# Kernel tuning notes

Measured on AMD Instinct MI355X. Metric: run time of the kernel, lower is better.

The kernel has to match this reference:

```python
import jax, jax.numpy as jnp
import numpy as np

S, B, C, H, E = 4096, 2, 256, 8, 131072
CC = C // H


def setup_inputs() -> dict:
    key = jax.random.key(0)
    ks = jax.random.split(key, 12)
    sc = 0.02
    inp = {
        "x": jax.random.normal(ks[0], (S, B, C), jnp.float32),
        "q_id": jax.random.randint(ks[1], (E,), 0, S, jnp.int32),
        "k_id": jax.random.randint(ks[2], (E,), 0, S, jnp.int32),
        "Wq": jax.random.normal(ks[3], (C, C), jnp.float32) * sc,
        "bq": jnp.zeros((C,), jnp.float32),
        "Wk": jax.random.normal(ks[4], (C, C), jnp.float32) * sc,
        "bk": jnp.zeros((C,), jnp.float32),
        "Wv": jax.random.normal(ks[5], (C, C), jnp.float32) * sc,
        "bv": jnp.zeros((C,), jnp.float32),
        "Wx": jax.random.normal(ks[6], (C, C), jnp.float32) * sc,
        "bx": jnp.zeros((C,), jnp.float32),
    }
    return inp


def reference(x, q_id, k_id, Wq, bq, Wk, bk, Wv, bv, Wx, bx):
    s, b, c = x.shape
    cc = c // H
    # qkv projections (torch Linear: x @ W.T + b)
    q = (x @ Wq.T + bq).reshape(s, b, H, cc)
    k = (x @ Wk.T + bk).reshape(s, b, H, cc)
    v = (x @ Wv.T + bv).reshape(s, b, H, cc)
    # per-edge scores: gather along sequence axis by edge ids
    qk = jnp.einsum('ebhc,ebhc->ebh', q[q_id], k[k_id])[..., None]  # [E,b,h,1]
    qk = qk / jnp.sqrt(jnp.asarray(cc, x.dtype))
    eqk = jnp.exp(qk - jnp.max(qk))  # global max, as in original
    # scatter-add softmax normalizer and weighted sum over edges
    d = jnp.zeros((s, b, H, 1), x.dtype).at[q_id].add(eqk)
    out = jnp.zeros((s, b, H, cc), x.dtype).at[q_id].add(eqk * v[k_id])
    out = (out / d).reshape(s, b, c)
    return out @ Wx.T + bx
```

## Files before the change

kernel.cpp:

```cpp
#include <hip/hip_runtime.h>

constexpr int S_  = 4096;
constexpr int B_  = 2;
constexpr int C_  = 256;
constexpr int H_  = 8;
constexpr int E_  = 131072;
constexpr int CC_ = 32;
constexpr int MR  = S_ * B_;

typedef __attribute__((ext_vector_type(8))) short bf16x8_t;
typedef __attribute__((ext_vector_type(4))) float f32x4_t;

__device__ __forceinline__ unsigned short f2bf(float f) {
    unsigned int u = __float_as_uint(f);
    u += 0x7fffu + ((u >> 16) & 1u);
    return (unsigned short)(u >> 16);
}
__device__ __forceinline__ float bflo(unsigned int u) { return __uint_as_float(u << 16); }
__device__ __forceinline__ float bfhi(unsigned int u) { return __uint_as_float(u & 0xffff0000u); }

__device__ __forceinline__ void cast8(const float* __restrict__ src, unsigned short* __restrict__ dst, int i) {
    const float4* s = (const float4*)src + (size_t)i * 2;
    float4 a = s[0], b = s[1];
    uint4 o;
    o.x = (unsigned)f2bf(a.x) | ((unsigned)f2bf(a.y) << 16);
    o.y = (unsigned)f2bf(a.z) | ((unsigned)f2bf(a.w) << 16);
    o.z = (unsigned)f2bf(b.x) | ((unsigned)f2bf(b.y) << 16);
    o.w = (unsigned)f2bf(b.z) | ((unsigned)f2bf(b.w) << 16);
    *((uint4*)dst + i) = o;
}


__global__ __launch_bounds__(256) void prep_kernel(
        const int* __restrict__ q_id, int* __restrict__ count,
        const float* __restrict__ x, unsigned short* __restrict__ xb,
        const float* __restrict__ Wq, const float* __restrict__ Wk,
        const float* __restrict__ Wv, const float* __restrict__ Wx,
        unsigned short* __restrict__ Wb) {
    const int bid = blockIdx.x, tid = threadIdx.x;
    if (bid < 512) {
        atomicAdd(&count[q_id[bid * 256 + tid]], 1);
    } else if (bid < 1536) {
        cast8(x, xb, (bid - 512) * 256 + tid);
    } else {
        int idx = bid - 1536;
        int z = idx >> 5;
        const float* src = (z == 0) ? Wq : (z == 1) ? Wk : (z == 2) ? Wv : Wx;
        cast8(src, Wb + (size_t)z * (C_ * C_), (idx & 31) * 256 + tid);
    }
}


__global__ __launch_bounds__(1024) void scan_kernel(const int* __restrict__ count,
                                                    int* __restrict__ base,
                                                    int* __restrict__ cursor) {
    __shared__ int wsums[16];
    const int t = threadIdx.x, lane = t & 63, w = t >> 6;
    int c0 = count[4 * t + 0], c1 = count[4 * t + 1];
    int c2 = count[4 * t + 2], c3 = count[4 * t + 3];
    int tsum = c0 + c1 + c2 + c3;
    int x = tsum;
#pragma unroll
    for (int off = 1; off < 64; off <<= 1) {
        int y = __shfl_up(x, off);
        if (lane >= off) x += y;
    }
    if (lane == 63) wsums[w] = x;
    __syncthreads();
    if (t == 0) {
        int run = 0;
#pragma unroll
        for (int i = 0; i < 16; ++i) { int v = wsums[i]; wsums[i] = run; run += v; }
        base[S_] = run;
    }
    __syncthreads();
    int excl = x - tsum + wsums[w];
    int b0 = excl, b1 = b0 + c0, b2 = b1 + c1, b3 = b2 + c2;
    base[4 * t + 0] = b0; base[4 * t + 1] = b1;
    base[4 * t + 2] = b2; base[4 * t + 3] = b3;
    cursor[4 * t + 0] = b0; cursor[4 * t + 1] = b1;
    cursor[4 * t + 2] = b2; cursor[4 * t + 3] = b3;
}


__global__ __launch_bounds__(256) void scatter_qkv_kernel(
        const int* __restrict__ q_id, const int* __restrict__ k_id,
        int* __restrict__ cursor, int* __restrict__ koff_sorted,
        const unsigned short* __restrict__ xb, const unsigned short* __restrict__ Wb,
        const float* __restrict__ bq, const float* __restrict__ bk, const float* __restrict__ bv,
        unsigned short* __restrict__ qb, unsigned short* __restrict__ kvb) {
    __shared__ __align__(16) unsigned short As[64][264];
    const int bid = blockIdx.x, tid = threadIdx.x;
    if (bid < 512) {
        int e = bid * 256 + tid;
        int pos = atomicAdd(&cursor[q_id[e]], 1);
        koff_sorted[pos] = k_id[e] << 10;
        return;
    }
    const int u = bid - 512;
    const int nb = u % 12, mg = u / 12;
    const int lane = tid & 63, wave = tid >> 6;
    const int l16 = lane & 15, quad = lane >> 4;
    const int z = nb >> 2;
    const int colz = ((nb & 3) << 6) + (wave << 4);

    const unsigned short* Wrow = Wb + (size_t)z * (C_ * C_) + (size_t)(colz + l16) * C_;
    bf16x8_t breg[8];
#pragma unroll
    for (int ks = 0; ks < 8; ++ks)
        breg[ks] = *(const bf16x8_t*)(Wrow + ks * 32 + quad * 8);

    const float* bias = (z == 0) ? bq : (z == 1) ? bk : bv;
    const float bcol = bias[colz + l16];
    unsigned short* ob = (z == 0) ? qb : kvb;
    const int ostr = (z == 0) ? 256 : 512;
    const int ocol = ((z == 2) ? 256 : 0) + colz + l16;

    const int c0 = (mg * 128) / 43, c1 = ((mg + 1) * 128) / 43;
    for (int c = c0; c < c1; ++c) {
        const int mbase = c * 64;
        __syncthreads();
#pragma unroll
        for (int it = 0; it < 8; ++it) {
            int l = it * 256 + tid;
            int r = l >> 5, cc = (l & 31) << 3;
            *(uint4*)&As[r][cc] = *(const uint4*)&xb[(size_t)(mbase + r) * C_ + cc];
        }
        __syncthreads();
#pragma unroll
        for (int mt = 0; mt < 4; ++mt) {
            f32x4_t acc = {0.f, 0.f, 0.f, 0.f};
#pragma unroll
            for (int ks = 0; ks < 8; ++ks) {
                bf16x8_t a = *(const bf16x8_t*)&As[mt * 16 + l16][ks * 32 + quad * 8];
                acc = __builtin_amdgcn_mfma_f32_16x16x32_bf16(a, breg[ks], acc, 0, 0, 0);
            }
            const int row0 = mbase + mt * 16 + quad * 4;
#pragma unroll
            for (int r = 0; r < 4; ++r)
                ob[(size_t)(row0 + r) * ostr + ocol] = f2bf(acc[r] + bcol);
        }
    }
}


__global__ __launch_bounds__(256) void attn_edge(
        const unsigned short* __restrict__ qb, const unsigned short* __restrict__ kvb,
        const int* __restrict__ base, const int* __restrict__ koff,
        unsigned short* __restrict__ attnb) {
    __shared__ float red[2][64][9];
    const int lane = threadIdx.x & 63;
    const int wave = threadIdx.x >> 6;
    const int rw = wave >> 1, part = wave & 1;
    const int s = blockIdx.x * 2 + rw;
    const int half = lane >> 5, hl = lane & 31;
    const int e0 = __builtin_amdgcn_readfirstlane(base[s]);
    const int e1 = __builtin_amdgcn_readfirstlane(base[s + 1]);

    const uint4 qq = *((const uint4*)(qb + (size_t)(s * 2 + half) * C_) + hl);
    const float q0 = bflo(qq.x), q1 = bfhi(qq.x), q2 = bflo(qq.y), q3 = bfhi(qq.y);
    const float q4 = bflo(qq.z), q5 = bfhi(qq.z), q6 = bflo(qq.w), q7 = bfhi(qq.w);

    float a0 = 0.f, a1 = 0.f, a2 = 0.f, a3 = 0.f, a4 = 0.f, a5 = 0.f, a6 = 0.f, a7 = 0.f;
    float wsum = 0.f;
    const float scale = 0.17677669529663687f;

    auto edge = [&](const uint4& kk, const uint4& vv) {
        float p = q0 * bflo(kk.x) + q1 * bfhi(kk.x)
                + q2 * bflo(kk.y) + q3 * bfhi(kk.y)
                + q4 * bflo(kk.z) + q5 * bfhi(kk.z)
                + q6 * bflo(kk.w) + q7 * bfhi(kk.w);
        p += __shfl_xor(p, 1);
        p += __shfl_xor(p, 2);
        const float w = __expf(p * scale);
        a0 = fmaf(w, bflo(vv.x), a0); a1 = fmaf(w, bfhi(vv.x), a1);
        a2 = fmaf(w, bflo(vv.y), a2); a3 = fmaf(w, bfhi(vv.y), a3);
        a4 = fmaf(w, bflo(vv.z), a4); a5 = fmaf(w, bfhi(vv.z), a5);
        a6 = fmaf(w, bflo(vv.w), a6); a7 = fmaf(w, bfhi(vv.w), a7);
        wsum += w;
    };
    auto fetch = [&](int my, int t, uint4& kk, uint4& vv) {
        int o = __builtin_amdgcn_readlane(my, part + 2 * t);
        const uint4* p = (const uint4*)(kvb + o + half * 512);
        kk = p[hl]; vv = p[32 + hl];
    };

    for (int b0 = e0; b0 < e1; b0 += 64) {
        const int m = min(64, e1 - b0);
        const int my = koff[b0 + ((lane < m) ? lane : 0)];
        const int nm = (m > part) ? ((m - part + 1) >> 1) : 0;
        uint4 kka = {}, vva = {}, kkb = {}, vvb = {};
        if (nm > 0) fetch(my, 0, kka, vva);
        if (nm > 1) fetch(my, 1, kkb, vvb);
        int t = 0;
        for (; t + 3 < nm; t += 2) {
            edge(kka, vva);
            fetch(my, t + 2, kka, vva);
            edge(kkb, vvb);
            fetch(my, t + 3, kkb, vvb);
        }
        if (t < nm)     edge(kka, vva);
        if (t + 1 < nm) edge(kkb, vvb);
        if (t + 2 < nm) { fetch(my, t + 2, kka, vva); edge(kka, vva); }
    }

    if (part == 1) {
        float* r = red[rw][lane];
        r[0] = a0; r[1] = a1; r[2] = a2; r[3] = a3;
        r[4] = a4; r[5] = a5; r[6] = a6; r[7] = a7; r[8] = wsum;
    }
    __syncthreads();
    if (part == 0) {
        const float* r = red[rw][lane];
        a0 += r[0]; a1 += r[1]; a2 += r[2]; a3 += r[3];
        a4 += r[4]; a5 += r[5]; a6 += r[6]; a7 += r[7]; wsum += r[8];
        const float inv = 1.0f / wsum;
        uint4 o;
        o.x = (unsigned)f2bf(a0 * inv) | ((unsigned)f2bf(a1 * inv) << 16);
        o.y = (unsigned)f2bf(a2 * inv) | ((unsigned)f2bf(a3 * inv) << 16);
        o.z = (unsigned)f2bf(a4 * inv) | ((unsigned)f2bf(a5 * inv) << 16);
        o.w = (unsigned)f2bf(a6 * inv) | ((unsigned)f2bf(a7 * inv) << 16);
        *((uint4*)(attnb + (size_t)(s * 2 + half) * C_) + hl) = o;
    }
}


__global__ __launch_bounds__(256) void gemm_proj(
        const unsigned short* __restrict__ attnb, const unsigned short* __restrict__ Wxb,
        const float* __restrict__ bx, float* __restrict__ out) {
    __shared__ __align__(16) unsigned short As[64][264];
    const int tid = threadIdx.x;
    const int nb = blockIdx.x & 3, mg = blockIdx.x >> 2;
    const int lane = tid & 63, wave = tid >> 6;
    const int l16 = lane & 15, quad = lane >> 4;
    const int colz = (nb << 6) + (wave << 4);

    const unsigned short* Wrow = Wxb + (size_t)(colz + l16) * C_;
    bf16x8_t breg[8];
#pragma unroll
    for (int ks = 0; ks < 8; ++ks)
        breg[ks] = *(const bf16x8_t*)(Wrow + ks * 32 + quad * 8);
    const float bcol = bx[colz + l16];
    const int ocol = colz + l16;

    const int mbase = mg * 64;
#pragma unroll
    for (int it = 0; it < 8; ++it) {
        int l = it * 256 + tid;
        int r = l >> 5, cc = (l & 31) << 3;
        *(uint4*)&As[r][cc] = *(const uint4*)&attnb[(size_t)(mbase + r) * C_ + cc];
    }
    __syncthreads();
#pragma unroll
    for (int mt = 0; mt < 4; ++mt) {
        f32x4_t acc = {0.f, 0.f, 0.f, 0.f};
#pragma unroll
        for (int ks = 0; ks < 8; ++ks) {
            bf16x8_t a = *(const bf16x8_t*)&As[mt * 16 + l16][ks * 32 + quad * 8];
            acc = __builtin_amdgcn_mfma_f32_16x16x32_bf16(a, breg[ks], acc, 0, 0, 0);
        }
        const int row0 = mbase + mt * 16 + quad * 4;
#pragma unroll
        for (int r = 0; r < 4; ++r)
            out[(size_t)(row0 + r) * C_ + ocol] = acc[r] + bcol;
    }
}


extern "C" void kernel_launch(void* const* d_in, const int* in_sizes, int n_in,
                              void* d_out, int out_size, void* d_ws, size_t ws_size,
                              hipStream_t stream) {
    const float* x  = (const float*)d_in[0];
    const int* q_id = (const int*)d_in[1];
    const int* k_id = (const int*)d_in[2];
    const float* Wq = (const float*)d_in[3];
    const float* bq = (const float*)d_in[4];
    const float* Wk = (const float*)d_in[5];
    const float* bk = (const float*)d_in[6];
    const float* Wv = (const float*)d_in[7];
    const float* bv = (const float*)d_in[8];
    const float* Wx = (const float*)d_in[9];
    const float* bx = (const float*)d_in[10];
    float* out = (float*)d_out;

    char* ws = (char*)d_ws;
    unsigned short* xb    = (unsigned short*)ws;                 ws += (size_t)MR * C_ * 2;
    unsigned short* qb    = (unsigned short*)ws;                 ws += (size_t)MR * C_ * 2;
    unsigned short* kvb   = (unsigned short*)ws;                 ws += (size_t)MR * 512 * 2;
    unsigned short* attnb = (unsigned short*)ws;                 ws += (size_t)MR * C_ * 2;
    unsigned short* Wb    = (unsigned short*)ws;                 ws += (size_t)4 * C_ * C_ * 2;
    int* count       = (int*)ws;                                 ws += S_ * 4;
    int* base        = (int*)ws;                                 ws += (S_ + 1) * 4;
    int* cursor      = (int*)ws;                                 ws += S_ * 4;
    int* koff_sorted = (int*)ws;

    hipMemsetAsync(count, 0, S_ * sizeof(int), stream);
    prep_kernel<<<1664, 256, 0, stream>>>(q_id, count, x, xb, Wq, Wk, Wv, Wx, Wb);
    scan_kernel<<<1, 1024, 0, stream>>>(count, base, cursor);
    scatter_qkv_kernel<<<1028, 256, 0, stream>>>(q_id, k_id, cursor, koff_sorted,
                                                 xb, Wb, bq, bk, bv, qb, kvb);
    attn_edge<<<S_ / 2, 256, 0, stream>>>(qb, kvb, base, koff_sorted, attnb);
    gemm_proj<<<512, 256, 0, stream>>>(attnb, Wb + (size_t)3 * C_ * C_, bx, out);
}
```

Before: 147.6 us.

## Store K in FP8, split K/V buffers, four waves per node in edge attention

Keys are now written in FP8 into their own buffer, and V gets a separate bf16 buffer, which shrinks the gathered K traffic per edge. The attention kernel now gives each sequence node one block of four waves instead of two waves. Each wave computes up to 16 edge weights first and then gathers V in a second pass, with a three-way shared-memory reduction at the end. The scan kernel is also reshaped to 256 threads with 16 elements each. FP8 keys add quantisation error to the attention scores, and the 16-entry weight array raises register pressure.

```diff
diff --git a/kernel.cpp b/kernel.cpp
--- a/kernel.cpp
+++ b/kernel.cpp
@@ -18,6 +18,44 @@
 }
 __device__ __forceinline__ float bflo(unsigned int u) { return __uint_as_float(u << 16); }
 __device__ __forceinline__ float bfhi(unsigned int u) { return __uint_as_float(u & 0xffff0000u); }
+
+__device__ __forceinline__ unsigned char f2fp8(float f) {
+#if __has_builtin(__builtin_amdgcn_cvt_pk_fp8_f32)
+    return (unsigned char)(__builtin_amdgcn_cvt_pk_fp8_f32(f, f, 0, false) & 0xff);
+#else
+    unsigned u = __float_as_uint(f);
+    unsigned s = (u >> 31) << 7;
+    int e = (int)((u >> 23) & 0xff) - 127;
+    unsigned m = u & 0x7fffff;
+    if (e < -9) return (unsigned char)s;
+    if (e < -6) {
+        float a = __uint_as_float(u & 0x7fffffff);
+        unsigned q = (unsigned)__float2int_rn(a * 512.0f);
+        return (unsigned char)(s | q);
+    }
+    unsigned mr = (m + 0x7ffffu + ((m >> 20) & 1u)) >> 20;
+    if (mr >= 8) { mr = 0; ++e; }
+    if (e > 8) return (unsigned char)(s | 0x7e);
+    return (unsigned char)(s | ((unsigned)(e + 7) << 3) | mr);
+#endif
+}
+
+__device__ __forceinline__ void fp8x4_dec(unsigned w, float* d) {
+#if __has_builtin(__builtin_amdgcn_cvt_pk_f32_fp8)
+    auto lo = __builtin_amdgcn_cvt_pk_f32_fp8((int)w, false);
+    auto hi = __builtin_amdgcn_cvt_pk_f32_fp8((int)w, true);
+    d[0] = lo[0]; d[1] = lo[1]; d[2] = hi[0]; d[3] = hi[1];
+#else
+#pragma unroll
+    for (int i = 0; i < 4; ++i) {
+        unsigned b = (w >> (8 * i)) & 0xffu;
+        unsigned s = b >> 7, e = (b >> 3) & 15u, m = b & 7u;
+        float v = e ? __uint_as_float(((e + 120u) << 23) | (m << 20))
+                    : (float)m * 0.001953125f;
+        d[i] = s ? -v : v;
+    }
+#endif
+}
 
 __device__ __forceinline__ void cast8(const float* __restrict__ src, unsigned short* __restrict__ dst, int i) {
     const float4* s = (const float4*)src + (size_t)i * 2;
@@ -51,15 +89,15 @@
 }
 
 
-__global__ __launch_bounds__(1024) void scan_kernel(const int* __restrict__ count,
-                                                    int* __restrict__ base,
-                                                    int* __restrict__ cursor) {
-    __shared__ int wsums[16];
+__global__ __launch_bounds__(256) void scan_kernel(const int* __restrict__ count,
+                                                   int* __restrict__ base,
+                                                   int* __restrict__ cursor) {
+    __shared__ int wsums[4];
     const int t = threadIdx.x, lane = t & 63, w = t >> 6;
-    int c0 = count[4 * t + 0], c1 = count[4 * t + 1];
-    int c2 = count[4 * t + 2], c3 = count[4 * t + 3];
-    int tsum = c0 + c1 + c2 + c3;
-    int x = tsum;
+    int c[16]; int s = 0;
+#pragma unroll
+    for (int i = 0; i < 16; ++i) { c[i] = count[t * 16 + i]; s += c[i]; }
+    int x = s;
 #pragma unroll
     for (int off = 1; off < 64; off <<= 1) {
         int y = __shfl_up(x, off);
@@ -70,89 +108,100 @@
     if (t == 0) {
         int run = 0;
 #pragma unroll
-        for (int i = 0; i < 16; ++i) { int v = wsums[i]; wsums[i] = run; run += v; }
+        for (int i = 0; i < 4; ++i) { int v = wsums[i]; wsums[i] = run; run += v; }
         base[S_] = run;
     }
     __syncthreads();
-    int excl = x - tsum + wsums[w];
-    int b0 = excl, b1 = b0 + c0, b2 = b1 + c1, b3 = b2 + c2;
-    base[4 * t + 0] = b0; base[4 * t + 1] = b1;
-    base[4 * t + 2] = b2; base[4 * t + 3] = b3;
-    cursor[4 * t + 0] = b0; cursor[4 * t + 1] = b1;
-    cursor[4 * t + 2] = b2; cursor[4 * t + 3] = b3;
+    int run = x - s + wsums[w];
+#pragma unroll
+    for (int i = 0; i < 16; ++i) {
+        base[t * 16 + i] = run; cursor[t * 16 + i] = run; run += c[i];
+    }
+}
+
+
+__device__ __forceinline__ void qkv_unit(
+        int u, int tid,
+        const unsigned short* __restrict__ xb, const unsigned short* __restrict__ Wb,
+        const float* __restrict__ bq, const float* __restrict__ bk, const float* __restrict__ bv,
+        unsigned short* __restrict__ qb, unsigned char* __restrict__ kf8,
+        unsigned short* __restrict__ vb, unsigned short (*As)[264]) {
+    const int nb = u % 12, mg = u / 12;
+    const int lane = tid & 63, wave = tid >> 6;
+    const int l16 = lane & 15, quad = lane >> 4;
+    const int z = nb >> 2;
+    const int colz = ((nb & 3) << 6) + (wave << 4);
+
+    const unsigned short* Wrow = Wb + (size_t)z * (C_ * C_) + (size_t)(colz + l16) * C_;
+    bf16x8_t breg[8];
+#pragma unroll
+    for (int ks = 0; ks < 8; ++ks)
+        breg[ks] = *(const bf16x8_t*)(Wrow + ks * 32 + quad * 8);
+
+    const float* bias = (z == 0) ? bq : (z == 1) ? bk : bv;
+    const float bcol = bias[colz + l16];
+    unsigned short* obb = (z == 0) ? qb : vb;
+    const int ocol = colz + l16;
+
+    const int c0 = (mg * 128) / 43, c1 = ((mg + 1) * 128) / 43;
+    for (int c = c0; c < c1; ++c) {
+        const int mbase = c * 64;
+        __syncthreads();
+#pragma unroll
+        for (int it = 0; it < 8; ++it) {
+            int l = it * 256 + tid;
+            int r = l >> 5, cc = (l & 31) << 3;
+            *(uint4*)&As[r][cc] = *(const uint4*)&xb[(size_t)(mbase + r) * C_ + cc];
+        }
+        __syncthreads();
+#pragma unroll
+        for (int mt = 0; mt < 4; ++mt) {
+            f32x4_t acc = {0.f, 0.f, 0.f, 0.f};
+#pragma unroll
+            for (int ks = 0; ks < 8; ++ks) {
+                bf16x8_t a = *(const bf16x8_t*)&As[mt * 16 + l16][ks * 32 + quad * 8];
+                acc = __builtin_amdgcn_mfma_f32_16x16x32_bf16(a, breg[ks], acc, 0, 0, 0);
+            }
+            const int row0 = mbase + mt * 16 + quad * 4;
+#pragma unroll
+            for (int r = 0; r < 4; ++r) {
+                float val = acc[r] + bcol;
+                if (z == 1) kf8[(size_t)(row0 + r) * 256 + ocol] = f2fp8(val);
+                else        obb[(size_t)(row0 + r) * 256 + ocol] = f2bf(val);
+            }
+        }
+    }
 }
 
 
 __global__ __launch_bounds__(256) void scatter_qkv_kernel(
         const int* __restrict__ q_id, const int* __restrict__ k_id,
-        int* __restrict__ cursor, int* __restrict__ koff_sorted,
+        int* __restrict__ cursor, int* __restrict__ koff,
         const unsigned short* __restrict__ xb, const unsigned short* __restrict__ Wb,
         const float* __restrict__ bq, const float* __restrict__ bk, const float* __restrict__ bv,
-        unsigned short* __restrict__ qb, unsigned short* __restrict__ kvb) {
+        unsigned short* __restrict__ qb, unsigned char* __restrict__ kf8,
+        unsigned short* __restrict__ vb) {
     __shared__ __align__(16) unsigned short As[64][264];
     const int bid = blockIdx.x, tid = threadIdx.x;
     if (bid < 512) {
         int e = bid * 256 + tid;
         int pos = atomicAdd(&cursor[q_id[e]], 1);
-        koff_sorted[pos] = k_id[e] << 10;
+        koff[pos] = k_id[e] << 9;
         return;
     }
-    const int u = bid - 512;
-    const int nb = u % 12, mg = u / 12;
-    const int lane = tid & 63, wave = tid >> 6;
-    const int l16 = lane & 15, quad = lane >> 4;
-    const int z = nb >> 2;
-    const int colz = ((nb & 3) << 6) + (wave << 4);
-
-    const unsigned short* Wrow = Wb + (size_t)z * (C_ * C_) + (size_t)(colz + l16) * C_;
-    bf16x8_t breg[8];
-#pragma unroll
-    for (int ks = 0; ks < 8; ++ks)
-        breg[ks] = *(const bf16x8_t*)(Wrow + ks * 32 + quad * 8);
-
-    const float* bias = (z == 0) ? bq : (z == 1) ? bk : bv;
-    const float bcol = bias[colz + l16];
-    unsigned short* ob = (z == 0) ? qb : kvb;
-    const int ostr = (z == 0) ? 256 : 512;
-    const int ocol = ((z == 2) ? 256 : 0) + colz + l16;
-
-    const int c0 = (mg * 128) / 43, c1 = ((mg + 1) * 128) / 43;
-    for (int c = c0; c < c1; ++c) {
-        const int mbase = c * 64;
-        __syncthreads();
-#pragma unroll
-        for (int it = 0; it < 8; ++it) {
-            int l = it * 256 + tid;
-            int r = l >> 5, cc = (l & 31) << 3;
-            *(uint4*)&As[r][cc] = *(const uint4*)&xb[(size_t)(mbase + r) * C_ + cc];
-        }
-        __syncthreads();
-#pragma unroll
-        for (int mt = 0; mt < 4; ++mt) {
-            f32x4_t acc = {0.f, 0.f, 0.f, 0.f};
-#pragma unroll
-            for (int ks = 0; ks < 8; ++ks) {
-                bf16x8_t a = *(const bf16x8_t*)&As[mt * 16 + l16][ks * 32 + quad * 8];
-                acc = __builtin_amdgcn_mfma_f32_16x16x32_bf16(a, breg[ks], acc, 0, 0, 0);
-            }
-            const int row0 = mbase + mt * 16 + quad * 4;
-#pragma unroll
-            for (int r = 0; r < 4; ++r)
-                ob[(size_t)(row0 + r) * ostr + ocol] = f2bf(acc[r] + bcol);
-        }
-    }
+    qkv_unit(bid - 512, tid, xb, Wb, bq, bk, bv, qb, kf8, vb, As);
 }
 
 
 __global__ __launch_bounds__(256) void attn_edge(
-        const unsigned short* __restrict__ qb, const unsigned short* __restrict__ kvb,
+        const unsigned short* __restrict__ qb, const unsigned char* __restrict__ kf8,
+        const unsigned short* __restrict__ vb,
         const int* __restrict__ base, const int* __restrict__ koff,
         unsigned short* __restrict__ attnb) {
-    __shared__ float red[2][64][9];
+    __shared__ float red[3][64][9];
     const int lane = threadIdx.x & 63;
-    const int wave = threadIdx.x >> 6;
-    const int rw = wave >> 1, part = wave & 1;
-    const int s = blockIdx.x * 2 + rw;
+    const int part = threadIdx.x >> 6;
+    const int s = blockIdx.x;
     const int half = lane >> 5, hl = lane & 31;
     const int e0 = __builtin_amdgcn_readfirstlane(base[s]);
     const int e1 = __builtin_amdgcn_readfirstlane(base[s + 1]);
@@ -164,56 +213,58 @@
     float a0 = 0.f, a1 = 0.f, a2 = 0.f, a3 = 0.f, a4 = 0.f, a5 = 0.f, a6 = 0.f, a7 = 0.f;
     float wsum = 0.f;
     const float scale = 0.17677669529663687f;
-
-    auto edge = [&](const uint4& kk, const uint4& vv) {
-        float p = q0 * bflo(kk.x) + q1 * bfhi(kk.x)
-                + q2 * bflo(kk.y) + q3 * bfhi(kk.y)
-                + q4 * bflo(kk.z) + q5 * bfhi(kk.z)
-                + q6 * bflo(kk.w) + q7 * bfhi(kk.w);
-        p += __shfl_xor(p, 1);
-        p += __shfl_xor(p, 2);
-        const float w = __expf(p * scale);
-        a0 = fmaf(w, bflo(vv.x), a0); a1 = fmaf(w, bfhi(vv.x), a1);
-        a2 = fmaf(w, bflo(vv.y), a2); a3 = fmaf(w, bfhi(vv.y), a3);
-        a4 = fmaf(w, bflo(vv.z), a4); a5 = fmaf(w, bfhi(vv.z), a5);
-        a6 = fmaf(w, bflo(vv.w), a6); a7 = fmaf(w, bfhi(vv.w), a7);
-        wsum += w;
-    };
-    auto fetch = [&](int my, int t, uint4& kk, uint4& vv) {
-        int o = __builtin_amdgcn_readlane(my, part + 2 * t);
-        const uint4* p = (const uint4*)(kvb + o + half * 512);
-        kk = p[hl]; vv = p[32 + hl];
-    };
-
-    for (int b0 = e0; b0 < e1; b0 += 64) {
-        const int m = min(64, e1 - b0);
-        const int my = koff[b0 + ((lane < m) ? lane : 0)];
-        const int nm = (m > part) ? ((m - part + 1) >> 1) : 0;
-        uint4 kka = {}, vva = {}, kkb = {}, vvb = {};
-        if (nm > 0) fetch(my, 0, kka, vva);
-        if (nm > 1) fetch(my, 1, kkb, vvb);
-        int t = 0;
-        for (; t + 3 < nm; t += 2) {
-            edge(kka, vva);
-            fetch(my, t + 2, kka, vva);
-            edge(kkb, vvb);
-            fetch(my, t + 3, kkb, vvb);
-        }
-        if (t < nm)     edge(kka, vva);
-        if (t + 1 < nm) edge(kkb, vvb);
-        if (t + 2 < nm) { fetch(my, t + 2, kka, vva); edge(kka, vva); }
-    }
-
-    if (part == 1) {
-        float* r = red[rw][lane];
+    const int hoff = half * 256;
+
+    for (int cb = e0; cb < e1; cb += 64) {
+        const int m = min(64, e1 - cb);
+        const int my = koff[cb + ((lane < m) ? lane : 0)];
+        const int nt = (m > part) ? ((m - part + 3) >> 2) : 0;
+        float wreg[16];
+#pragma unroll
+        for (int t = 0; t < 16; ++t) {
+            wreg[t] = 0.f;
+            if (t < nt) {
+                const int o = __shfl(my, part + 4 * t);
+                const uint2 kk = *(const uint2*)(kf8 + o + hoff + hl * 8);
+                float kd[8];
+                fp8x4_dec(kk.x, kd);
+                fp8x4_dec(kk.y, kd + 4);
+                float p = q0 * kd[0] + q1 * kd[1] + q2 * kd[2] + q3 * kd[3]
+                        + q4 * kd[4] + q5 * kd[5] + q6 * kd[6] + q7 * kd[7];
+                p += __shfl_xor(p, 1);
+                p += __shfl_xor(p, 2);
+                const float w = __expf(p * scale);
+                wreg[t] = w;
+                wsum += w;
+            }
+        }
+#pragma unroll
+        for (int t = 0; t < 16; ++t) {
+            if (t < nt) {
+                const int o = __shfl(my, part + 4 * t);
+                const uint4 vv = *(const uint4*)(vb + o + hoff + hl * 8);
+                const float w = wreg[t];
+                a0 = fmaf(w, bflo(vv.x), a0); a1 = fmaf(w, bfhi(vv.x), a1);
+                a2 = fmaf(w, bflo(vv.y), a2); a3 = fmaf(w, bfhi(vv.y), a3);
+                a4 = fmaf(w, bflo(vv.z), a4); a5 = fmaf(w, bfhi(vv.z), a5);
+                a6 = fmaf(w, bflo(vv.w), a6); a7 = fmaf(w, bfhi(vv.w), a7);
+            }
+        }
+    }
+
+    if (part) {
+        float* r = &red[part - 1][lane][0];
         r[0] = a0; r[1] = a1; r[2] = a2; r[3] = a3;
         r[4] = a4; r[5] = a5; r[6] = a6; r[7] = a7; r[8] = wsum;
     }
     __syncthreads();
     if (part == 0) {
-        const float* r = red[rw][lane];
-        a0 += r[0]; a1 += r[1]; a2 += r[2]; a3 += r[3];
-        a4 += r[4]; a5 += r[5]; a6 += r[6]; a7 += r[7]; wsum += r[8];
+#pragma unroll
+        for (int pp = 0; pp < 3; ++pp) {
+            const float* r = &red[pp][lane][0];
+            a0 += r[0]; a1 += r[1]; a2 += r[2]; a3 += r[3];
+            a4 += r[4]; a5 += r[5]; a6 += r[6]; a7 += r[7]; wsum += r[8];
+        }
         const float inv = 1.0f / wsum;
         uint4 o;
         o.x = (unsigned)f2bf(a0 * inv) | ((unsigned)f2bf(a1 * inv) << 16);
@@ -284,21 +335,22 @@
     float* out = (float*)d_out;
 
     char* ws = (char*)d_ws;
-    unsigned short* xb    = (unsigned short*)ws;                 ws += (size_t)MR * C_ * 2;
-    unsigned short* qb    = (unsigned short*)ws;                 ws += (size_t)MR * C_ * 2;
-    unsigned short* kvb   = (unsigned short*)ws;                 ws += (size_t)MR * 512 * 2;
-    unsigned short* attnb = (unsigned short*)ws;                 ws += (size_t)MR * C_ * 2;
-    unsigned short* Wb    = (unsigned short*)ws;                 ws += (size_t)4 * C_ * C_ * 2;
-    int* count       = (int*)ws;                                 ws += S_ * 4;
-    int* base        = (int*)ws;                                 ws += (S_ + 1) * 4;
-    int* cursor      = (int*)ws;                                 ws += S_ * 4;
-    int* koff_sorted = (int*)ws;
+    unsigned short* xb    = (unsigned short*)ws;   ws += (size_t)MR * C_ * 2;
+    unsigned short* qb    = (unsigned short*)ws;   ws += (size_t)MR * C_ * 2;
+    unsigned char*  kf8   = (unsigned char*)ws;    ws += (size_t)MR * C_;
+    unsigned short* vb    = (unsigned short*)ws;   ws += (size_t)MR * C_ * 2;
+    unsigned short* attnb = (unsigned short*)ws;   ws += (size_t)MR * C_ * 2;
+    unsigned short* Wb    = (unsigned short*)ws;   ws += (size_t)4 * C_ * C_ * 2;
+    int* count  = (int*)ws;                        ws += S_ * 4;
+    int* base   = (int*)ws;                        ws += (S_ + 1) * 4;
+    int* cursor = (int*)ws;                        ws += S_ * 4;
+    int* koff   = (int*)ws;
 
     hipMemsetAsync(count, 0, S_ * sizeof(int), stream);
     prep_kernel<<<1664, 256, 0, stream>>>(q_id, count, x, xb, Wq, Wk, Wv, Wx, Wb);
-    scan_kernel<<<1, 1024, 0, stream>>>(count, base, cursor);
-    scatter_qkv_kernel<<<1028, 256, 0, stream>>>(q_id, k_id, cursor, koff_sorted,
-                                                 xb, Wb, bq, bk, bv, qb, kvb);
-    attn_edge<<<S_ / 2, 256, 0, stream>>>(qb, kvb, base, koff_sorted, attnb);
+    scan_kernel<<<1, 256, 0, stream>>>(count, base, cursor);
+    scatter_qkv_kernel<<<1028, 256, 0, stream>>>(q_id, k_id, cursor, koff,
+                                                 xb, Wb, bq, bk, bv, qb, kf8, vb);
+    attn_edge<<<S_, 256, 0, stream>>>(qb, kf8, vb, base, koff, attnb);
     gemm_proj<<<512, 256, 0, stream>>>(attnb, Wb + (size_t)3 * C_ * C_, bx, out);
 }
```

New measurement: 148.4 us. About the same (+0.5%).
